# Optimization experiments

Measured on AMD Instinct MI355X. Metric: run time of the kernel, lower is better.

Reference implementation:

```python
import jax, jax.numpy as jnp
import numpy as np

N_NODES = 50000
N_EDGES = 800000
NUM_GRAPHS = 64
F_IN, F_HID, F_HID2, F_OUT = 128, 96, 48, 32


def gcn_conv(x, W, b, src, dst, n_nodes):
    # PyG GCNConv: h = x @ W; out = D^{-1/2} (A+I) D^{-1/2} h + b
    # src/dst already include self loops; degree computed on dst.
    h = x @ W  # [N, F_out]
    deg = jax.ops.segment_sum(jnp.ones(dst.shape[0], dtype=h.dtype), dst, num_segments=n_nodes)
    dinv = jax.lax.rsqrt(deg)  # deg >= 1 due to self loops
    norm = dinv[src] * dinv[dst]  # [E]
    msg = h[src] * norm[:, None]  # gather + scale
    out = jax.ops.segment_sum(msg, dst, num_segments=n_nodes)  # scatter-add
    return out + b


def setup_inputs() -> dict:
    key = jax.random.key(0)
    ks = jax.random.split(key, 10)
    x = jax.random.normal(ks[0], (N_NODES, F_IN), dtype=jnp.float32)
    edge_index = jax.random.randint(ks[1], (2, N_EDGES), 0, N_NODES, dtype=jnp.int64)
    batch = jnp.sort(jax.random.randint(ks[2], (N_NODES,), 0, NUM_GRAPHS, dtype=jnp.int64))
    def glorot(k, fi, fo):
        s = np.sqrt(6.0 / (fi + fo)).astype(np.float32)
        return jax.random.uniform(k, (fi, fo), dtype=jnp.float32, minval=-s, maxval=s)
    W1 = glorot(ks[3], F_IN, F_HID)
    b1 = jnp.zeros((F_HID,), dtype=jnp.float32)
    W2 = glorot(ks[4], F_HID, F_HID2)
    b2 = jnp.zeros((F_HID2,), dtype=jnp.float32)
    W3 = glorot(ks[5], F_HID2, F_OUT)
    b3 = jnp.zeros((F_OUT,), dtype=jnp.float32)
    return {"x": x, "edge_index": edge_index, "batch": batch,
            "W1": W1, "b1": b1, "W2": W2, "b2": b2, "W3": W3, "b3": b3}


def reference(x, edge_index, batch, W1, b1, W2, b2, W3, b3):
    n = x.shape[0]
    loops = jnp.arange(n, dtype=edge_index.dtype)
    src = jnp.concatenate([edge_index[0], loops])
    dst = jnp.concatenate([edge_index[1], loops])

    h = jax.nn.relu(gcn_conv(x, W1, b1, src, dst, n))
    h = jax.nn.relu(gcn_conv(h, W2, b2, src, dst, n))
    h = jax.nn.relu(gcn_conv(h, W3, b3, src, dst, n))

    # global mean pool over graphs in the batch
    sums = jax.ops.segment_sum(h, batch, num_segments=NUM_GRAPHS)
    cnt = jax.ops.segment_sum(jnp.ones((n,), dtype=h.dtype), batch, num_segments=NUM_GRAPHS)
    return sums / jnp.maximum(cnt, 1.0)[:, None]
```

## Files before the change

kernel.cpp:

```cpp
#include <hip/hip_runtime.h>

#define N_NODES 50000
#define N_EDGES 800000
#define NUM_GRAPHS 64

#define CAPLOG 6
#define CAP    (1 << CAPLOG)
#define ZROW   N_NODES

__device__ __forceinline__ float bf_lo(unsigned u) { return __uint_as_float(u << 16); }
__device__ __forceinline__ float bf_hi(unsigned u) { return __uint_as_float(u & 0xffff0000u); }
__device__ __forceinline__ unsigned short f2bf(float f) {
    unsigned u = __float_as_uint(f);
    return (unsigned short)((u + 0x7fffu + ((u >> 16) & 1u)) >> 16);
}

template<int S>
__device__ __forceinline__ void agg_row8(const unsigned short* __restrict__ Hc,
                                         const unsigned short* __restrict__ csr,
                                         int node, int m, float a[8]) {
    uint4 sv = *(const uint4*)(Hc + (size_t)node * S);
    a[0] = bf_lo(sv.x); a[1] = bf_hi(sv.x); a[2] = bf_lo(sv.y); a[3] = bf_hi(sv.y);
    a[4] = bf_lo(sv.z); a[5] = bf_hi(sv.z); a[6] = bf_lo(sv.w); a[7] = bf_hi(sv.w);
    const int e0 = node << CAPLOG, e1 = e0 + m;
    for (int e = e0; e < e1; e += 4) {
        ushort4 ss = *(const ushort4*)&csr[e];
        int s0 = ss.x;
        int s1 = (e + 1 < e1) ? (int)ss.y : ZROW;
        int s2 = (e + 2 < e1) ? (int)ss.z : ZROW;
        int s3 = (e + 3 < e1) ? (int)ss.w : ZROW;
        uint4 v0 = *(const uint4*)(Hc + (size_t)s0 * S);
        uint4 v1 = *(const uint4*)(Hc + (size_t)s1 * S);
        uint4 v2 = *(const uint4*)(Hc + (size_t)s2 * S);
        uint4 v3 = *(const uint4*)(Hc + (size_t)s3 * S);
        a[0] += bf_lo(v0.x) + bf_lo(v1.x) + bf_lo(v2.x) + bf_lo(v3.x);
        a[1] += bf_hi(v0.x) + bf_hi(v1.x) + bf_hi(v2.x) + bf_hi(v3.x);
        a[2] += bf_lo(v0.y) + bf_lo(v1.y) + bf_lo(v2.y) + bf_lo(v3.y);
        a[3] += bf_hi(v0.y) + bf_hi(v1.y) + bf_hi(v2.y) + bf_hi(v3.y);
        a[4] += bf_lo(v0.z) + bf_lo(v1.z) + bf_lo(v2.z) + bf_lo(v3.z);
        a[5] += bf_hi(v0.z) + bf_hi(v1.z) + bf_hi(v2.z) + bf_hi(v3.z);
        a[6] += bf_lo(v0.w) + bf_lo(v1.w) + bf_lo(v2.w) + bf_lo(v3.w);
        a[7] += bf_hi(v0.w) + bf_hi(v1.w) + bf_hi(v2.w) + bf_hi(v3.w);
    }
}

#define SC_NG    4
#define SC_BPG   256
#define SC_GRID  (SC_NG * SC_BPG)
#define NPG      ((N_NODES + SC_NG - 1) / SC_NG)
__global__ __launch_bounds__(256) void k_scatter_xcd(
        const int* __restrict__ ei, int* __restrict__ cnt,
        unsigned short* __restrict__ csr,
        const int* __restrict__ batch, int* __restrict__ start) {
    if (blockIdx.x == SC_GRID) {
        int t = threadIdx.x;
        if (t <= NUM_GRAPHS) {
            int lo = 0, hi = N_NODES;
            while (lo < hi) {
                int mid = (lo + hi) >> 1;
                if (batch[mid] < t) lo = mid + 1; else hi = mid;
            }
            start[t] = lo;
        }
        return;
    }
    const int g  = blockIdx.x & (SC_NG - 1);
    const int b  = blockIdx.x / SC_NG;
    const int lo = g * NPG, hi = lo + NPG;
    const int* __restrict__ dst = ei + N_EDGES;
    for (int e = b * 256 + threadIdx.x; e < N_EDGES; e += 256 * SC_BPG) {
        int d = dst[e];
        if (d >= lo && d < hi) {
            int old = atomicAdd(&cnt[d], 1);
            if (old < CAP) csr[(d << CAPLOG) + old] = (unsigned short)ei[e];
        }
    }
}

template <int K, int M, int MT, int FTH, int NTH, int NT, int OSTRIDE>
__global__ __launch_bounds__(FTH * NTH)
void k_gemm(const float* __restrict__ X, const float* __restrict__ W,
            const int* __restrict__ cnt, unsigned short* __restrict__ H) {
    constexpr int BLOCK = FTH * NTH;
    __shared__ float ws[K * MT];
    const int tid = threadIdx.x;
    const int n0 = blockIdx.x * (NTH * NT);
    const int c0 = blockIdx.y * MT;

    if (blockIdx.x == 0 && blockIdx.y == 0 && tid < M / 4) {
        ushort4 z = make_ushort4(0, 0, 0, 0);
        *(ushort4*)&H[(size_t)ZROW * OSTRIDE + tid * 4] = z;
    }

    for (int i = tid; i < K * MT / 4; i += BLOCK) {
        int k = i / (MT / 4), cv = i % (MT / 4);
        *(float4*)&ws[k * MT + cv * 4] = *(const float4*)&W[k * M + c0 + cv * 4];
    }
    __syncthreads();

    const int ft = tid % FTH;
    const int nt = tid / FTH;
    const float* xp[NT];
    #pragma unroll
    for (int i = 0; i < NT; ++i) {
        int node = n0 + nt * NT + i;
        int nc = node < N_NODES ? node : N_NODES - 1;
        xp[i] = X + (size_t)nc * K;
    }
    float acc[NT][4];
    #pragma unroll
    for (int i = 0; i < NT; ++i) { acc[i][0] = acc[i][1] = acc[i][2] = acc[i][3] = 0.f; }

    for (int k = 0; k < K; k += 4) {
        float4 w0 = *(const float4*)&ws[(k + 0) * MT + ft * 4];
        float4 w1 = *(const float4*)&ws[(k + 1) * MT + ft * 4];
        float4 w2 = *(const float4*)&ws[(k + 2) * MT + ft * 4];
        float4 w3 = *(const float4*)&ws[(k + 3) * MT + ft * 4];
        #pragma unroll
        for (int i = 0; i < NT; ++i) {
            float4 xv = *(const float4*)(xp[i] + k);
            acc[i][0] += xv.x * w0.x + xv.y * w1.x + xv.z * w2.x + xv.w * w3.x;
            acc[i][1] += xv.x * w0.y + xv.y * w1.y + xv.z * w2.y + xv.w * w3.y;
            acc[i][2] += xv.x * w0.z + xv.y * w1.z + xv.z * w2.z + xv.w * w3.z;
            acc[i][3] += xv.x * w0.w + xv.y * w1.w + xv.z * w2.w + xv.w * w3.w;
        }
    }
    #pragma unroll
    for (int i = 0; i < NT; ++i) {
        int node = n0 + nt * NT + i;
        if (node < N_NODES) {
            float s = rsqrtf((float)(cnt[node] + 1));
            ushort4 o;
            o.x = f2bf(acc[i][0] * s); o.y = f2bf(acc[i][1] * s);
            o.z = f2bf(acc[i][2] * s); o.w = f2bf(acc[i][3] * s);
            *(ushort4*)&H[(size_t)node * OSTRIDE + c0 + ft * 4] = o;
        }
    }
}

__global__ __launch_bounds__(384) void k_agg12(
        const unsigned short* __restrict__ H1, const int* __restrict__ cnt,
        const unsigned short* __restrict__ csr, const float* __restrict__ b1,
        const float* __restrict__ W2, unsigned short* __restrict__ H2) {
    __shared__ float Ws[96 * 48];
    __shared__ float T[32][97];
    __shared__ float dinvS[32];
    const int t = threadIdx.x;
    for (int i = t; i < 1152; i += 384)
        *(float4*)&Ws[i * 4] = *(const float4*)&W2[i * 4];

    if (blockIdx.x == 0 && t < 16) {
        ushort4 z = make_ushort4(0, 0, 0, 0);
        *(ushort4*)&H2[(size_t)ZROW * 64 + t * 4] = z;
    }

    const int n_l = t / 12, c = t % 12;
    const int node = blockIdx.x * 32 + n_l;
    if (node < N_NODES) {
        int deg = cnt[node];
        float d = rsqrtf((float)(deg + 1));
        if (c == 0) dinvS[n_l] = d;
        float a[8];
        agg_row8<96>(H1 + c * 8, csr, node, min(deg, CAP), a);
        const float4* bp = (const float4*)(b1 + c * 8);
        float4 b0 = bp[0], bb1 = bp[1];
        float* Tr = &T[n_l][c * 8];
        Tr[0] = fmaxf(a[0] * d + b0.x, 0.f);  Tr[1] = fmaxf(a[1] * d + b0.y, 0.f);
        Tr[2] = fmaxf(a[2] * d + b0.z, 0.f);  Tr[3] = fmaxf(a[3] * d + b0.w, 0.f);
        Tr[4] = fmaxf(a[4] * d + bb1.x, 0.f); Tr[5] = fmaxf(a[5] * d + bb1.y, 0.f);
        Tr[6] = fmaxf(a[6] * d + bb1.z, 0.f); Tr[7] = fmaxf(a[7] * d + bb1.w, 0.f);
    }
    __syncthreads();

    const int n2 = t / 12;
    const int f0 = (t % 12) * 4;
    const int gn = blockIdx.x * 32 + n2;
    if (gn < N_NODES) {
        float4 acc = make_float4(0.f, 0.f, 0.f, 0.f);
        for (int k = 0; k < 96; ++k) {
            float tv = T[n2][k];
            float4 wv = *(const float4*)&Ws[k * 48 + f0];
            acc.x += tv * wv.x; acc.y += tv * wv.y; acc.z += tv * wv.z; acc.w += tv * wv.w;
        }
        float s2 = dinvS[n2];
        ushort4 o;
        o.x = f2bf(acc.x * s2); o.y = f2bf(acc.y * s2);
        o.z = f2bf(acc.z * s2); o.w = f2bf(acc.w * s2);
        *(ushort4*)&H2[(size_t)gn * 64 + f0] = o;
    }
}

__global__ __launch_bounds__(384) void k_agg23(
        const unsigned short* __restrict__ H2, const int* __restrict__ cnt,
        const unsigned short* __restrict__ csr, const float* __restrict__ b2,
        const float* __restrict__ W3, unsigned short* __restrict__ H3) {
    __shared__ float Ws[48 * 32];
    __shared__ float T[64][49];
    __shared__ float dinvS[64];
    const int t = threadIdx.x;
    for (int i = t; i < 384; i += 384)
        *(float4*)&Ws[i * 4] = *(const float4*)&W3[i * 4];

    if (blockIdx.x == 0 && t < 8) {
        ushort4 z = make_ushort4(0, 0, 0, 0);
        *(ushort4*)&H3[(size_t)ZROW * 32 + t * 4] = z;
    }

    const int n_l = t / 6, c = t % 6;
    const int node = blockIdx.x * 64 + n_l;
    if (node < N_NODES) {
        int deg = cnt[node];
        float d = rsqrtf((float)(deg + 1));
        if (c == 0) dinvS[n_l] = d;
        float a[8];
        agg_row8<64>(H2 + c * 8, csr, node, min(deg, CAP), a);
        const float4* bp = (const float4*)(b2 + c * 8);
        float4 b0 = bp[0], bb1 = bp[1];
        float* Tr = &T[n_l][c * 8];
        Tr[0] = fmaxf(a[0] * d + b0.x, 0.f);  Tr[1] = fmaxf(a[1] * d + b0.y, 0.f);
        Tr[2] = fmaxf(a[2] * d + b0.z, 0.f);  Tr[3] = fmaxf(a[3] * d + b0.w, 0.f);
        Tr[4] = fmaxf(a[4] * d + bb1.x, 0.f); Tr[5] = fmaxf(a[5] * d + bb1.y, 0.f);
        Tr[6] = fmaxf(a[6] * d + bb1.z, 0.f); Tr[7] = fmaxf(a[7] * d + bb1.w, 0.f);
    }
    __syncthreads();

    for (int vid = t; vid < 512; vid += 384) {
        const int n2 = vid / 8;
        const int f0 = (vid % 8) * 4;
        const int gn = blockIdx.x * 64 + n2;
        if (gn < N_NODES) {
            float4 acc = make_float4(0.f, 0.f, 0.f, 0.f);
            for (int k = 0; k < 48; ++k) {
                float tv = T[n2][k];
                float4 wv = *(const float4*)&Ws[k * 32 + f0];
                acc.x += tv * wv.x; acc.y += tv * wv.y; acc.z += tv * wv.z; acc.w += tv * wv.w;
            }
            float s3 = dinvS[n2];
            ushort4 o;
            o.x = f2bf(acc.x * s3); o.y = f2bf(acc.y * s3);
            o.z = f2bf(acc.z * s3); o.w = f2bf(acc.w * s3);
            *(ushort4*)&H3[(size_t)gn * 32 + f0] = o;
        }
    }
}

__global__ __launch_bounds__(256) void k_agg3p(
        const unsigned short* __restrict__ H3, const int* __restrict__ cnt,
        const unsigned short* __restrict__ csr, const float* __restrict__ b3,
        const int* __restrict__ batch, const int* __restrict__ start,
        float* __restrict__ gsum) {
    __shared__ float T[64][33];
    __shared__ float R[8][32];
    const int t = threadIdx.x;
    const int base = blockIdx.x * 64;

    const int n_l = t / 4, c = t % 4;
    const int node = base + n_l;
    if (node < N_NODES) {
        int deg = cnt[node];
        float d = rsqrtf((float)(deg + 1));
        float a[8];
        agg_row8<32>(H3 + c * 8, csr, node, min(deg, CAP), a);
        const float4* bp = (const float4*)(b3 + c * 8);
        float4 b0 = bp[0], b1 = bp[1];
        float* Tr = &T[n_l][c * 8];
        Tr[0] = fmaxf(a[0] * d + b0.x, 0.f); Tr[1] = fmaxf(a[1] * d + b0.y, 0.f);
        Tr[2] = fmaxf(a[2] * d + b0.z, 0.f); Tr[3] = fmaxf(a[3] * d + b0.w, 0.f);
        Tr[4] = fmaxf(a[4] * d + b1.x, 0.f); Tr[5] = fmaxf(a[5] * d + b1.y, 0.f);
        Tr[6] = fmaxf(a[6] * d + b1.z, 0.f); Tr[7] = fmaxf(a[7] * d + b1.w, 0.f);
    }
    __syncthreads();

    const int g_lo = batch[base < N_NODES ? base : N_NODES - 1];
    const int last = base + 63 < N_NODES ? base + 63 : N_NODES - 1;
    const int g_hi = batch[last];
    const int f = t & 31, k = t >> 5;
    for (int g = g_lo; g <= g_hi; ++g) {
        int r_lo = start[g] - base;     if (r_lo < 0) r_lo = 0;
        int r_hi = start[g + 1] - base; if (r_hi > 64) r_hi = 64;
        float p = 0.f;
        for (int r = r_lo + k; r < r_hi; r += 8) p += T[r][f];
        R[k][f] = p;
        __syncthreads();
        if (k == 0) {
            float s = R[0][f] + R[1][f] + R[2][f] + R[3][f]
                    + R[4][f] + R[5][f] + R[6][f] + R[7][f];
            if (r_hi > r_lo) atomicAdd(&gsum[g * 32 + f], s);
        }
        __syncthreads();
    }
}

__global__ void k_final(const float* __restrict__ gsum, const int* __restrict__ start,
                        float* __restrict__ out) {
    int t = blockIdx.x * blockDim.x + threadIdx.x;
    if (t < NUM_GRAPHS * 32) {
        int g = t >> 5;
        float c = (float)(start[g + 1] - start[g]);
        out[t] = gsum[t] / fmaxf(c, 1.0f);
    }
}

extern "C" void kernel_launch(void* const* d_in, const int* in_sizes, int n_in,
                              void* d_out, int out_size, void* d_ws, size_t ws_size,
                              hipStream_t stream) {
    const float* x     = (const float*)d_in[0];
    const int*   ei    = (const int*)d_in[1];
    const int*   batch = (const int*)d_in[2];
    const float* W1    = (const float*)d_in[3];
    const float* b1    = (const float*)d_in[4];
    const float* W2    = (const float*)d_in[5];
    const float* b2    = (const float*)d_in[6];
    const float* W3    = (const float*)d_in[7];
    const float* b3    = (const float*)d_in[8];
    float* out = (float*)d_out;

    char* ws = (char*)d_ws;
    size_t o = 0;
    auto alloc = [&](size_t bytes) {
        char* p = ws + o;
        o = (o + bytes + 255) & ~(size_t)255;
        return p;
    };
    unsigned short* H1 = (unsigned short*)alloc((size_t)(N_NODES + 1) * 96 * 2);
    unsigned short* H2 = (unsigned short*)alloc((size_t)(N_NODES + 1) * 64 * 2);
    unsigned short* H3 = (unsigned short*)alloc((size_t)(N_NODES + 1) * 32 * 2);
    int*   cnt    = (int*)alloc((size_t)N_NODES * 4);
    unsigned short* csr = (unsigned short*)alloc((size_t)N_NODES * CAP * 2);
    int*   start  = (int*)alloc((NUM_GRAPHS + 1) * 4);
    float* gsum   = (float*)alloc((size_t)NUM_GRAPHS * 32 * 4);

    hipMemsetAsync(cnt, 0, (size_t)N_NODES * 4, stream);
    hipMemsetAsync(gsum, 0, (size_t)NUM_GRAPHS * 32 * 4, stream);

    hipLaunchKernelGGL(k_scatter_xcd, dim3(SC_GRID + 1), dim3(256), 0, stream, ei, cnt, csr, batch, start);
    hipLaunchKernelGGL((k_gemm<128, 96, 48, 12, 16, 4, 96>), dim3((N_NODES + 63) / 64, 2), dim3(192), 0, stream,
                       x, W1, cnt, H1);
    hipLaunchKernelGGL(k_agg12, dim3((N_NODES + 31) / 32), dim3(384), 0, stream,
                       H1, cnt, csr, b1, W2, H2);
    hipLaunchKernelGGL(k_agg23, dim3((N_NODES + 63) / 64), dim3(384), 0, stream,
                       H2, cnt, csr, b2, W3, H3);
    hipLaunchKernelGGL(k_agg3p, dim3((N_NODES + 63) / 64), dim3(256), 0, stream,
                       H3, cnt, csr, b3, batch, start, gsum);
    hipLaunchKernelGGL(k_final, dim3((NUM_GRAPHS * 32 + 255) / 256), dim3(256), 0, stream,
                       gsum, start, out);
}
```

Baseline: 218.7 us.

## Build CSR via bucketed counting sort instead of global atomic scatter

Replaces the single scatter kernel, which does global atomics on per-node counters and makes four passes over the edges, with a two-level bucket sort. The new pipeline is a per-block bucket histogram, a scan, a bucketing pass that writes (src,dst) pairs, and a per-bucket CSR fill that uses shared-memory atomics. The goal is to cut global atomic contention and the random writes into the CSR. In exchange it adds three kernel launches, a serial single-block scan, and an extra round trip of the edge pairs through memory.

```diff
diff --git a/kernel.cpp b/kernel.cpp
--- a/kernel.cpp
+++ b/kernel.cpp
@@ -7,6 +7,11 @@
 #define CAPLOG 6
 #define CAP    (1 << CAPLOG)
 #define ZROW   N_NODES
+
+#define BSH    8
+#define NBUK   ((N_NODES + 255) >> 8)
+#define NB     256
+#define EPB    (N_EDGES / NB)
 
 __device__ __forceinline__ float bf_lo(unsigned u) { return __uint_as_float(u << 16); }
 __device__ __forceinline__ float bf_hi(unsigned u) { return __uint_as_float(u & 0xffff0000u); }
@@ -44,15 +49,10 @@
     }
 }
 
-#define SC_NG    4
-#define SC_BPG   256
-#define SC_GRID  (SC_NG * SC_BPG)
-#define NPG      ((N_NODES + SC_NG - 1) / SC_NG)
-__global__ __launch_bounds__(256) void k_scatter_xcd(
-        const int* __restrict__ ei, int* __restrict__ cnt,
-        unsigned short* __restrict__ csr,
+__global__ __launch_bounds__(256) void k_hist(
+        const int* __restrict__ ei, int* __restrict__ hist,
         const int* __restrict__ batch, int* __restrict__ start) {
-    if (blockIdx.x == SC_GRID) {
+    if (blockIdx.x == NB) {
         int t = threadIdx.x;
         if (t <= NUM_GRAPHS) {
             int lo = 0, hi = N_NODES;
@@ -64,17 +64,73 @@
         }
         return;
     }
-    const int g  = blockIdx.x & (SC_NG - 1);
-    const int b  = blockIdx.x / SC_NG;
-    const int lo = g * NPG, hi = lo + NPG;
+    __shared__ int h[NBUK];
+    const int t = threadIdx.x, b = blockIdx.x;
+    for (int i = t; i < NBUK; i += 256) h[i] = 0;
+    __syncthreads();
     const int* __restrict__ dst = ei + N_EDGES;
-    for (int e = b * 256 + threadIdx.x; e < N_EDGES; e += 256 * SC_BPG) {
+    const int e0 = b * EPB;
+    for (int e = e0 + t; e < e0 + EPB; e += 256)
+        atomicAdd(&h[dst[e] >> BSH], 1);
+    __syncthreads();
+    for (int i = t; i < NBUK; i += 256) hist[i * NB + b] = h[i];
+}
+
+__global__ __launch_bounds__(256) void k_scan(
+        int* __restrict__ hist, int* __restrict__ bucketStart) {
+    __shared__ int tot[NBUK];
+    const int k = threadIdx.x;
+    if (k < NBUK) {
+        int s = 0;
+        int* row = hist + k * NB;
+        #pragma unroll 4
+        for (int b = 0; b < NB; ++b) { int v = row[b]; row[b] = s; s += v; }
+        tot[k] = s;
+    }
+    __syncthreads();
+    if (k == 0) {
+        int s = 0;
+        for (int i = 0; i < NBUK; ++i) { bucketStart[i] = s; s += tot[i]; }
+        bucketStart[NBUK] = s;
+    }
+}
+
+__global__ __launch_bounds__(256) void k_bucket(
+        const int* __restrict__ ei, const int* __restrict__ hist,
+        const int* __restrict__ bucketStart, ushort2* __restrict__ pairs) {
+    __shared__ int cur[NBUK];
+    const int t = threadIdx.x, b = blockIdx.x;
+    for (int i = t; i < NBUK; i += 256)
+        cur[i] = bucketStart[i] + hist[i * NB + b];
+    __syncthreads();
+    const int* __restrict__ src = ei;
+    const int* __restrict__ dst = ei + N_EDGES;
+    const int e0 = b * EPB;
+    for (int e = e0 + t; e < e0 + EPB; e += 256) {
         int d = dst[e];
-        if (d >= lo && d < hi) {
-            int old = atomicAdd(&cnt[d], 1);
-            if (old < CAP) csr[(d << CAPLOG) + old] = (unsigned short)ei[e];
-        }
-    }
+        int p = atomicAdd(&cur[d >> BSH], 1);
+        pairs[p] = make_ushort2((unsigned short)src[e], (unsigned short)d);
+    }
+}
+
+__global__ __launch_bounds__(256) void k_csr(
+        const ushort2* __restrict__ pairs, const int* __restrict__ bucketStart,
+        int* __restrict__ cnt, unsigned short* __restrict__ csr) {
+    __shared__ int lc[256];
+    const int t = threadIdx.x, k = blockIdx.x;
+    lc[t] = 0;
+    __syncthreads();
+    const int base = k << BSH;
+    const int p0 = bucketStart[k], p1 = bucketStart[k + 1];
+    for (int p = p0 + t; p < p1; p += 256) {
+        ushort2 sd = pairs[p];
+        int d = sd.y;
+        int old = atomicAdd(&lc[d - base], 1);
+        if (old < CAP) csr[((size_t)d << CAPLOG) + old] = sd.x;
+    }
+    __syncthreads();
+    const int n = base + t;
+    if (n < N_NODES) cnt[n] = lc[t];
 }
 
 template <int K, int M, int MT, int FTH, int NTH, int NT, int OSTRIDE>
@@ -329,11 +385,16 @@
     unsigned short* csr = (unsigned short*)alloc((size_t)N_NODES * CAP * 2);
     int*   start  = (int*)alloc((NUM_GRAPHS + 1) * 4);
     float* gsum   = (float*)alloc((size_t)NUM_GRAPHS * 32 * 4);
-
-    hipMemsetAsync(cnt, 0, (size_t)N_NODES * 4, stream);
+    int*   hist   = (int*)alloc((size_t)NBUK * NB * 4);
+    int*   bstart = (int*)alloc((NBUK + 1) * 4);
+    ushort2* pairs = (ushort2*)alloc((size_t)N_EDGES * 4);
+
     hipMemsetAsync(gsum, 0, (size_t)NUM_GRAPHS * 32 * 4, stream);
 
-    hipLaunchKernelGGL(k_scatter_xcd, dim3(SC_GRID + 1), dim3(256), 0, stream, ei, cnt, csr, batch, start);
+    hipLaunchKernelGGL(k_hist, dim3(NB + 1), dim3(256), 0, stream, ei, hist, batch, start);
+    hipLaunchKernelGGL(k_scan, dim3(1), dim3(256), 0, stream, hist, bstart);
+    hipLaunchKernelGGL(k_bucket, dim3(NB), dim3(256), 0, stream, ei, hist, bstart, pairs);
+    hipLaunchKernelGGL(k_csr, dim3(NBUK), dim3(256), 0, stream, pairs, bstart, cnt, csr);
     hipLaunchKernelGGL((k_gemm<128, 96, 48, 12, 16, 4, 96>), dim3((N_NODES + 63) / 64, 2), dim3(192), 0, stream,
                        x, W1, cnt, H1);
     hipLaunchKernelGGL(k_agg12, dim3((N_NODES + 31) / 32), dim3(384), 0, stream,
```

Result: slower. 226.4 us (+3.5%).

## Run edge scatter and first GEMM concurrently in one fused launch

Applied to the files above, without the earlier changes.

Merges the CSR-building scatter kernel and the first-layer GEMM into a single grid whose blocks pick a role by block index, so the atomic-bound scatter and the compute-bound GEMM can overlap. Because the GEMM no longer waits for degree counts, it writes unscaled fp32 output, and a new scale kernel then applies the degree normalisation and converts to bf16. This adds an extra fp32 write and read of the full hidden matrix plus one more launch, and the scatter blocks drop from 256 to 192 threads.

```diff
diff --git a/kernel.cpp b/kernel.cpp
--- a/kernel.cpp
+++ b/kernel.cpp
@@ -48,76 +48,77 @@
 #define SC_BPG   256
 #define SC_GRID  (SC_NG * SC_BPG)
 #define NPG      ((N_NODES + SC_NG - 1) / SC_NG)
-__global__ __launch_bounds__(256) void k_scatter_xcd(
+#define GEMM_NBX ((N_NODES + 63) / 64)
+#define GEMM_NB  (GEMM_NBX * 2)
+#define FUSE_GRID (SC_GRID + 1 + GEMM_NB)
+
+__global__ __launch_bounds__(192) void k_scatgemm(
         const int* __restrict__ ei, int* __restrict__ cnt,
         unsigned short* __restrict__ csr,
-        const int* __restrict__ batch, int* __restrict__ start) {
-    if (blockIdx.x == SC_GRID) {
-        int t = threadIdx.x;
-        if (t <= NUM_GRAPHS) {
+        const int* __restrict__ batch, int* __restrict__ start,
+        const float* __restrict__ X, const float* __restrict__ W,
+        float* __restrict__ Hraw) {
+    const int bid = blockIdx.x;
+    const int tid = threadIdx.x;
+
+    if (bid < SC_GRID) {
+        const int g  = bid & (SC_NG - 1);
+        const int b  = bid / SC_NG;
+        const int lo = g * NPG, hi = lo + NPG;
+        const int* __restrict__ dst = ei + N_EDGES;
+        for (int e = b * 192 + tid; e < N_EDGES; e += 192 * SC_BPG) {
+            int d = dst[e];
+            if (d >= lo && d < hi) {
+                int old = atomicAdd(&cnt[d], 1);
+                if (old < CAP) csr[(d << CAPLOG) + old] = (unsigned short)ei[e];
+            }
+        }
+        return;
+    }
+    if (bid == SC_GRID) {
+        if (tid <= NUM_GRAPHS) {
             int lo = 0, hi = N_NODES;
             while (lo < hi) {
                 int mid = (lo + hi) >> 1;
-                if (batch[mid] < t) lo = mid + 1; else hi = mid;
+                if (batch[mid] < tid) lo = mid + 1; else hi = mid;
             }
-            start[t] = lo;
+            start[tid] = lo;
         }
         return;
     }
-    const int g  = blockIdx.x & (SC_NG - 1);
-    const int b  = blockIdx.x / SC_NG;
-    const int lo = g * NPG, hi = lo + NPG;
-    const int* __restrict__ dst = ei + N_EDGES;
-    for (int e = b * 256 + threadIdx.x; e < N_EDGES; e += 256 * SC_BPG) {
-        int d = dst[e];
-        if (d >= lo && d < hi) {
-            int old = atomicAdd(&cnt[d], 1);
-            if (old < CAP) csr[(d << CAPLOG) + old] = (unsigned short)ei[e];
-        }
-    }
-}
-
-template <int K, int M, int MT, int FTH, int NTH, int NT, int OSTRIDE>
-__global__ __launch_bounds__(FTH * NTH)
-void k_gemm(const float* __restrict__ X, const float* __restrict__ W,
-            const int* __restrict__ cnt, unsigned short* __restrict__ H) {
-    constexpr int BLOCK = FTH * NTH;
-    __shared__ float ws[K * MT];
-    const int tid = threadIdx.x;
-    const int n0 = blockIdx.x * (NTH * NT);
-    const int c0 = blockIdx.y * MT;
-
-    if (blockIdx.x == 0 && blockIdx.y == 0 && tid < M / 4) {
-        ushort4 z = make_ushort4(0, 0, 0, 0);
-        *(ushort4*)&H[(size_t)ZROW * OSTRIDE + tid * 4] = z;
-    }
-
-    for (int i = tid; i < K * MT / 4; i += BLOCK) {
-        int k = i / (MT / 4), cv = i % (MT / 4);
-        *(float4*)&ws[k * MT + cv * 4] = *(const float4*)&W[k * M + c0 + cv * 4];
+
+    const int gb = bid - SC_GRID - 1;
+    const int bx = gb % GEMM_NBX;
+    const int by = gb / GEMM_NBX;
+    const int n0 = bx * 64;
+    const int c0 = by * 48;
+    __shared__ float ws[128 * 48];
+    for (int i = tid; i < 128 * 48 / 4; i += 192) {
+        int k = i / 12, cv = i % 12;
+        *(float4*)&ws[k * 48 + cv * 4] = *(const float4*)&W[k * 96 + c0 + cv * 4];
     }
     __syncthreads();
 
-    const int ft = tid % FTH;
-    const int nt = tid / FTH;
-    const float* xp[NT];
+    const int ft = tid % 12;
+    const int nt = tid / 12;
+    const float* xp[4];
     #pragma unroll
-    for (int i = 0; i < NT; ++i) {
-        int node = n0 + nt * NT + i;
+    for (int i = 0; i < 4; ++i) {
+        int node = n0 + nt * 4 + i;
         int nc = node < N_NODES ? node : N_NODES - 1;
-        xp[i] = X + (size_t)nc * K;
-    }
-    float acc[NT][4];
+        xp[i] = X + (size_t)nc * 128;
+    }
+    float acc[4][4];
     #pragma unroll
-    for (int i = 0; i < NT; ++i) { acc[i][0] = acc[i][1] = acc[i][2] = acc[i][3] = 0.f; }
-
-    for (int k = 0; k < K; k += 4) {
-        float4 w0 = *(const float4*)&ws[(k + 0) * MT + ft * 4];
-        float4 w1 = *(const float4*)&ws[(k + 1) * MT + ft * 4];
-        float4 w2 = *(const float4*)&ws[(k + 2) * MT + ft * 4];
-        float4 w3 = *(const float4*)&ws[(k + 3) * MT + ft * 4];
+    for (int i = 0; i < 4; ++i) { acc[i][0] = acc[i][1] = acc[i][2] = acc[i][3] = 0.f; }
+
+    for (int k = 0; k < 128; k += 4) {
+        float4 w0 = *(const float4*)&ws[(k + 0) * 48 + ft * 4];
+        float4 w1 = *(const float4*)&ws[(k + 1) * 48 + ft * 4];
+        float4 w2 = *(const float4*)&ws[(k + 2) * 48 + ft * 4];
+        float4 w3 = *(const float4*)&ws[(k + 3) * 48 + ft * 4];
         #pragma unroll
-        for (int i = 0; i < NT; ++i) {
+        for (int i = 0; i < 4; ++i) {
             float4 xv = *(const float4*)(xp[i] + k);
             acc[i][0] += xv.x * w0.x + xv.y * w1.x + xv.z * w2.x + xv.w * w3.x;
             acc[i][1] += xv.x * w0.y + xv.y * w1.y + xv.z * w2.y + xv.w * w3.y;
@@ -126,15 +127,30 @@
         }
     }
     #pragma unroll
-    for (int i = 0; i < NT; ++i) {
-        int node = n0 + nt * NT + i;
-        if (node < N_NODES) {
-            float s = rsqrtf((float)(cnt[node] + 1));
-            ushort4 o;
-            o.x = f2bf(acc[i][0] * s); o.y = f2bf(acc[i][1] * s);
-            o.z = f2bf(acc[i][2] * s); o.w = f2bf(acc[i][3] * s);
-            *(ushort4*)&H[(size_t)node * OSTRIDE + c0 + ft * 4] = o;
-        }
+    for (int i = 0; i < 4; ++i) {
+        int node = n0 + nt * 4 + i;
+        if (node < N_NODES)
+            *(float4*)&Hraw[(size_t)node * 96 + c0 + ft * 4] =
+                make_float4(acc[i][0], acc[i][1], acc[i][2], acc[i][3]);
+    }
+}
+
+__global__ __launch_bounds__(256) void k_scale(
+        const float* __restrict__ Hraw, const int* __restrict__ cnt,
+        unsigned short* __restrict__ H1) {
+    const int NQ = (N_NODES + 1) * 24;
+    for (int q = blockIdx.x * 256 + threadIdx.x; q < NQ; q += gridDim.x * 256) {
+        int n = q / 24, c = (q % 24) * 4;
+        if (n == ZROW) {
+            *(ushort4*)&H1[(size_t)n * 96 + c] = make_ushort4(0, 0, 0, 0);
+            continue;
+        }
+        float s = rsqrtf((float)(cnt[n] + 1));
+        float4 v = *(const float4*)&Hraw[(size_t)n * 96 + c];
+        ushort4 o;
+        o.x = f2bf(v.x * s); o.y = f2bf(v.y * s);
+        o.z = f2bf(v.z * s); o.w = f2bf(v.w * s);
+        *(ushort4*)&H1[(size_t)n * 96 + c] = o;
     }
 }
 
@@ -325,6 +341,7 @@
     unsigned short* H1 = (unsigned short*)alloc((size_t)(N_NODES + 1) * 96 * 2);
     unsigned short* H2 = (unsigned short*)alloc((size_t)(N_NODES + 1) * 64 * 2);
     unsigned short* H3 = (unsigned short*)alloc((size_t)(N_NODES + 1) * 32 * 2);
+    float* H1raw  = (float*)alloc((size_t)N_NODES * 96 * 4);
     int*   cnt    = (int*)alloc((size_t)N_NODES * 4);
     unsigned short* csr = (unsigned short*)alloc((size_t)N_NODES * CAP * 2);
     int*   start  = (int*)alloc((NUM_GRAPHS + 1) * 4);
@@ -333,9 +350,9 @@
     hipMemsetAsync(cnt, 0, (size_t)N_NODES * 4, stream);
     hipMemsetAsync(gsum, 0, (size_t)NUM_GRAPHS * 32 * 4, stream);
 
-    hipLaunchKernelGGL(k_scatter_xcd, dim3(SC_GRID + 1), dim3(256), 0, stream, ei, cnt, csr, batch, start);
-    hipLaunchKernelGGL((k_gemm<128, 96, 48, 12, 16, 4, 96>), dim3((N_NODES + 63) / 64, 2), dim3(192), 0, stream,
-                       x, W1, cnt, H1);
+    hipLaunchKernelGGL(k_scatgemm, dim3(FUSE_GRID), dim3(192), 0, stream,
+                       ei, cnt, csr, batch, start, x, W1, H1raw);
+    hipLaunchKernelGGL(k_scale, dim3(2048), dim3(256), 0, stream, H1raw, cnt, H1);
     hipLaunchKernelGGL(k_agg12, dim3((N_NODES + 31) / 32), dim3(384), 0, stream,
                        H1, cnt, csr, b1, W2, H2);
     hipLaunchKernelGGL(k_agg23, dim3((N_NODES + 63) / 64), dim3(384), 0, stream,
```

After: 214.7 us. No clear change (-1.8%).
